# Performance work log

Measured on AMD Instinct MI355X. Metric: run time of the kernel, lower is better.

## Reference

```python
import jax, jax.numpy as jnp
import numpy as np


def setup_inputs() -> dict:
    key = jax.random.key(0)
    k1, k2 = jax.random.split(key)
    B, Ld, Lq, D = 32, 2048, 512, 256
    doc = jax.random.normal(k1, (B, Ld, D), dtype=jnp.float32)
    query = jax.random.normal(k2, (B, Lq, D), dtype=jnp.float32)
    doc_mask = jnp.ones((B, Ld), dtype=jnp.float32)
    q_mask = jnp.ones((B, Lq), dtype=jnp.float32)
    return {"doc": doc, "query": query, "doc_mask": doc_mask, "q_mask": q_mask}


def reference(doc, query, doc_mask, q_mask):
    # match_score: [B, Lq, Ld] = tanh(query @ doc^T)
    match_score = jnp.tanh(jnp.einsum('bqd,btd->bqt', query, doc))
    # sum over query positions -> [B, Ld]; softmax over doc positions
    query_to_doc_att = jax.nn.softmax(jnp.sum(match_score, axis=1), axis=-1)
    # sum over doc positions -> [B, Lq]; softmax over query positions
    doc_to_query_att = jax.nn.softmax(jnp.sum(match_score, axis=-1), axis=-1)
    # mask and renormalize
    alpha = query_to_doc_att * doc_mask
    alpha = alpha / jnp.sum(alpha, axis=1, keepdims=True)
    beta = doc_to_query_att * q_mask
    beta = beta / jnp.sum(beta, axis=1, keepdims=True)
    # weighted pooling: doc^T @ alpha -> [B, D]; query^T @ beta -> [B, D]
    doc_vector = jnp.einsum('btd,bt->bd', doc, alpha)
    que_vector = jnp.einsum('bqd,bq->bd', query, beta)
    return jnp.concatenate([doc_vector, que_vector], axis=1)  # [B, 2D]
```

## Files before the change

kernel.cpp:

```cpp
#include <hip/hip_runtime.h>
#include <hip/hip_bf16.h>
#include <cstdint>

#define BB 32
#define LD 2048
#define LQ 512
#define DD 256
#define BM 128
#define BN 128
#define BK 64

typedef _Float16 half8 __attribute__((ext_vector_type(8)));
typedef _Float16 half4 __attribute__((ext_vector_type(4)));
typedef float float4v __attribute__((ext_vector_type(4)));

__device__ __forceinline__ float tanh_fast(float x) {
    float t = __builtin_amdgcn_exp2f(x * 2.885390081777927f);
    float r = __builtin_amdgcn_rcpf(t + 1.0f);
    return fmaf(-2.0f, r, 1.0f);
}

__device__ __forceinline__ void load_lds16(const void* g, void* s) {
    __builtin_amdgcn_global_load_lds((const __attribute__((address_space(1))) void*)g,
                                     (__attribute__((address_space(3))) void*)s, 16, 0, 0);
}

#define DOCN8 (BB * LD * DD / 8)
#define QRYN8 (BB * LQ * DD / 8)

__global__ __launch_bounds__(256) void kconv(const float* __restrict__ doc,
                                             const float* __restrict__ qry,
                                             _Float16* __restrict__ dh,
                                             _Float16* __restrict__ qh) {
    int i = blockIdx.x * 256 + threadIdx.x;
    const float* src;
    _Float16* dst;
    int idx;
    if (i < DOCN8) { src = doc; dst = dh; idx = i; }
    else           { src = qry; dst = qh; idx = i - DOCN8; }
    const float4v* s = (const float4v*)src + (size_t)idx * 2;
    float4v a = s[0], c = s[1];
    half8 h = {(_Float16)a[0], (_Float16)a[1], (_Float16)a[2], (_Float16)a[3],
               (_Float16)c[0], (_Float16)c[1], (_Float16)c[2], (_Float16)c[3]};
    *((half8*)dst + idx) = h;
}

template <bool F16SRC>
__global__ __launch_bounds__(256) void k1(const void* __restrict__ qsrc,
                                          const void* __restrict__ dsrc,
                                          float* __restrict__ pa,
                                          float* __restrict__ pb) {
    __shared__ _Float16 sQ[BM * BK];
    __shared__ _Float16 sD[BN * BK];
    __shared__ float srow[BM][2];
    __shared__ float scol[BN][2];
    const int bq = blockIdx.x, bt = blockIdx.y, b = blockIdx.z;
    const int tid = threadIdx.x;
    const int lane = tid & 63;
    const int wave = tid >> 6;
    const int r16 = lane & 15;
    const int q4 = lane >> 4;
    const int mb = (wave >> 1) * 64, nb = (wave & 1) * 64;

    float4v acc[4][4];
    float4v zero = {0.f, 0.f, 0.f, 0.f};
#pragma unroll
    for (int m = 0; m < 4; m++)
#pragma unroll
        for (int n = 0; n < 4; n++) acc[m][n] = zero;

    const int lrow = lane >> 3;
    const int lcol = ((lane & 7) ^ lrow) * 8;

    for (int kk = 0; kk < DD; kk += BK) {
        __syncthreads();
        if constexpr (F16SRC) {
            const _Float16* Qh = (const _Float16*)qsrc + ((size_t)b * LQ + bq * BM) * DD;
            const _Float16* Dh = (const _Float16*)dsrc + ((size_t)b * LD + bt * BN) * DD;
#pragma unroll
            for (int j = 0; j < 4; j++) {
                int c = wave * 4 + j;
                int row = 8 * c + lrow;
                load_lds16(Qh + (size_t)row * DD + kk + lcol, &sQ[c * 512]);
                load_lds16(Dh + (size_t)row * DD + kk + lcol, &sD[c * 512]);
            }
        } else {
            const float* Qf = (const float*)qsrc + ((size_t)b * LQ + bq * BM) * DD;
            const float* Df = (const float*)dsrc + ((size_t)b * LD + bt * BN) * DD;
#pragma unroll
            for (int i = 0; i < 8; i++) {
                int f = tid + 256 * i;
                int row = f >> 4, c = f & 15;
                int c2 = c >> 1, hlf = c & 1;
                int p = c2 ^ (row & 7);
                float4v v = *(const float4v*)(Qf + (size_t)row * DD + kk + 4 * c);
                half4 h = {(_Float16)v[0], (_Float16)v[1], (_Float16)v[2], (_Float16)v[3]};
                *(half4*)(&sQ[row * BK + p * 8 + hlf * 4]) = h;
                float4v w = *(const float4v*)(Df + (size_t)row * DD + kk + 4 * c);
                half4 h2 = {(_Float16)w[0], (_Float16)w[1], (_Float16)w[2], (_Float16)w[3]};
                *(half4*)(&sD[row * BK + p * 8 + hlf * 4]) = h2;
            }
        }
        __syncthreads();

#pragma unroll
        for (int kk2 = 0; kk2 < 2; kk2++) {
            const int sw = ((4 * kk2 + q4) ^ (r16 & 7)) * 8;
            half8 af[4], bf[4];
#pragma unroll
            for (int m = 0; m < 4; m++) af[m] = *(const half8*)(&sQ[(mb + 16 * m + r16) * BK + sw]);
#pragma unroll
            for (int n = 0; n < 4; n++) bf[n] = *(const half8*)(&sD[(nb + 16 * n + r16) * BK + sw]);
#pragma unroll
            for (int m = 0; m < 4; m++)
#pragma unroll
                for (int n = 0; n < 4; n++)
                    acc[m][n] = __builtin_amdgcn_mfma_f32_16x16x32_f16(af[m], bf[n], acc[m][n], 0, 0, 0);
        }
    }

    float rsum[4][4];
    float csum[4];
#pragma unroll
    for (int m = 0; m < 4; m++)
#pragma unroll
        for (int r = 0; r < 4; r++) rsum[m][r] = 0.f;
#pragma unroll
    for (int n = 0; n < 4; n++) csum[n] = 0.f;

#pragma unroll
    for (int m = 0; m < 4; m++)
#pragma unroll
        for (int n = 0; n < 4; n++) {
            float t0 = tanh_fast(acc[m][n][0]);
            float t1 = tanh_fast(acc[m][n][1]);
            float t2 = tanh_fast(acc[m][n][2]);
            float t3 = tanh_fast(acc[m][n][3]);
            csum[n] += t0 + t1 + t2 + t3;
            rsum[m][0] += t0;
            rsum[m][1] += t1;
            rsum[m][2] += t2;
            rsum[m][3] += t3;
        }

#pragma unroll
    for (int m = 0; m < 4; m++) {
#pragma unroll
        for (int r = 0; r < 4; r++) {
            float v = rsum[m][r];
            v += __shfl_xor(v, 1);
            v += __shfl_xor(v, 2);
            v += __shfl_xor(v, 4);
            v += __shfl_xor(v, 8);
            rsum[m][r] = v;
        }
        if (r16 < 4) {
            float v = (r16 == 0) ? rsum[m][0] : (r16 == 1) ? rsum[m][1] : (r16 == 2) ? rsum[m][2] : rsum[m][3];
            srow[mb + 16 * m + 4 * q4 + r16][wave & 1] = v;
        }
    }
#pragma unroll
    for (int n = 0; n < 4; n++) {
        float v = csum[n];
        v += __shfl_xor(v, 16);
        v += __shfl_xor(v, 32);
        if (lane < 16) scol[nb + 16 * n + lane][wave >> 1] = v;
    }
    __syncthreads();
    if (tid < 128) {
        float v = srow[tid][0] + srow[tid][1];
        pb[((size_t)bt * BB + b) * LQ + bq * BM + tid] = v;
        float u = scol[tid][0] + scol[tid][1];
        pa[((size_t)bq * BB + b) * LD + bt * BN + tid] = u;
    }
}

__global__ __launch_bounds__(256) void k2(const float* __restrict__ pa, const float* __restrict__ pb,
                                          const float* __restrict__ dmask, const float* __restrict__ qmask,
                                          float* __restrict__ alpha, float* __restrict__ beta,
                                          float* __restrict__ out) {
    __shared__ float sl[2048];
    __shared__ float sm[4], ss[4];
    int blk = blockIdx.x, tid = threadIdx.x, lane = tid & 63, wave = tid >> 6;
    const float* mk;
    float* dst;
    int n;
    if (blk < BB) {
        int b = blk;
        out[b * 2 * DD + tid] = 0.f;
        out[b * 2 * DD + 256 + tid] = 0.f;
        n = LD;
        mk = dmask + b * LD;
        dst = alpha + b * LD;
        for (int i = tid; i < n; i += 256) {
            float s = 0.f;
#pragma unroll
            for (int j = 0; j < 4; j++) s += pa[((size_t)j * BB + b) * LD + i];
            sl[i] = s;
        }
    } else {
        int b = blk - BB;
        n = LQ;
        mk = qmask + b * LQ;
        dst = beta + b * LQ;
        for (int i = tid; i < n; i += 256) {
            float s = 0.f;
#pragma unroll
            for (int j = 0; j < 16; j++) s += pb[((size_t)j * BB + b) * LQ + i];
            sl[i] = s;
        }
    }
    __syncthreads();
    float mx = -3.0e38f;
    for (int i = tid; i < n; i += 256) mx = fmaxf(mx, sl[i]);
#pragma unroll
    for (int s = 1; s < 64; s <<= 1) mx = fmaxf(mx, __shfl_xor(mx, s));
    if (lane == 0) sm[wave] = mx;
    __syncthreads();
    mx = fmaxf(fmaxf(sm[0], sm[1]), fmaxf(sm[2], sm[3]));
    const float L2E = 1.4426950408889634f;
    float sum = 0.f;
    for (int i = tid; i < n; i += 256) {
        float e = __builtin_amdgcn_exp2f((sl[i] - mx) * L2E) * mk[i];
        sl[i] = e;
        sum += e;
    }
#pragma unroll
    for (int s = 1; s < 64; s <<= 1) sum += __shfl_xor(sum, s);
    if (lane == 0) ss[wave] = sum;
    __syncthreads();
    sum = ss[0] + ss[1] + ss[2] + ss[3];
    float inv = 1.0f / sum;
    for (int i = tid; i < n; i += 256) dst[i] = sl[i] * inv;
}

template <bool F16SRC>
__global__ __launch_bounds__(256) void k3(const float* __restrict__ docf, const float* __restrict__ qryf,
                                          const _Float16* __restrict__ dh, const _Float16* __restrict__ qh,
                                          const float* __restrict__ alpha, const float* __restrict__ beta,
                                          float* __restrict__ out) {
    __shared__ float sm[8 * DD];
    int blk = blockIdx.x, tid = threadIdx.x;
    const float* srcf;
    const _Float16* srch;
    const float* w;
    float* dst;
    if (blk < BB * 16) {
        int b = blk >> 4, ch = blk & 15;
        srcf = docf + ((size_t)b * LD + ch * 128) * DD;
        srch = dh + ((size_t)b * LD + ch * 128) * DD;
        w = alpha + b * LD + ch * 128;
        dst = out + b * 2 * DD;
    } else {
        int k = blk - BB * 16;
        int b = k >> 2, ch = k & 3;
        srcf = qryf + ((size_t)b * LQ + ch * 128) * DD;
        srch = qh + ((size_t)b * LQ + ch * 128) * DD;
        w = beta + b * LQ + ch * 128;
        dst = out + b * 2 * DD + DD;
    }
    int g = tid >> 5, c = tid & 31;
    float acc[8];
#pragma unroll
    for (int j = 0; j < 8; j++) acc[j] = 0.f;
#pragma unroll
    for (int r = 0; r < 16; r++) {
        int t = r * 8 + g;
        float wt = w[t];
        if constexpr (F16SRC) {
            half8 x = *(const half8*)(srch + (size_t)t * DD + c * 8);
#pragma unroll
            for (int j = 0; j < 8; j++) acc[j] += wt * (float)x[j];
        } else {
            const float4v* p = (const float4v*)(srcf + (size_t)t * DD + c * 8);
            float4v x0 = p[0], x1 = p[1];
#pragma unroll
            for (int j = 0; j < 4; j++) { acc[j] += wt * x0[j]; acc[4 + j] += wt * x1[j]; }
        }
    }
#pragma unroll
    for (int j = 0; j < 8; j++) sm[g * DD + c * 8 + j] = acc[j];
    __syncthreads();
    float s = 0.f;
#pragma unroll
    for (int g2 = 0; g2 < 8; g2++) s += sm[g2 * DD + tid];
    atomicAdd(dst + tid, s);
}

extern "C" void kernel_launch(void* const* d_in, const int* in_sizes, int n_in,
                              void* d_out, int out_size, void* d_ws, size_t ws_size,
                              hipStream_t stream) {
    (void)in_sizes; (void)n_in; (void)out_size;
    const float* doc = (const float*)d_in[0];
    const float* qry = (const float*)d_in[1];
    const float* dmask = (const float*)d_in[2];
    const float* qmask = (const float*)d_in[3];
    float* out = (float*)d_out;

    float* pa = (float*)d_ws;
    float* pb = pa + 4 * BB * LD;
    float* alpha = pb + 16 * BB * LQ;
    float* beta = alpha + BB * LD;
    _Float16* dh = (_Float16*)(beta + BB * LQ);
    _Float16* qh = dh + (size_t)BB * LD * DD;
    size_t needed = (size_t)(4 * BB * LD + 16 * BB * LQ + BB * LD + BB * LQ) * 4 +
                    ((size_t)BB * LD * DD + (size_t)BB * LQ * DD) * 2;
    bool useF16 = ws_size >= needed;

    if (useF16) {
        kconv<<<(DOCN8 + QRYN8) / 256, 256, 0, stream>>>(doc, qry, dh, qh);
        k1<true><<<dim3(LQ / BM, LD / BN, BB), 256, 0, stream>>>(qh, dh, pa, pb);
    } else {
        k1<false><<<dim3(LQ / BM, LD / BN, BB), 256, 0, stream>>>(qry, doc, pa, pb);
    }
    k2<<<2 * BB, 256, 0, stream>>>(pa, pb, dmask, qmask, alpha, beta, out);
    if (useF16) {
        k3<true><<<BB * 16 + BB * 4, 256, 0, stream>>>(doc, qry, dh, qh, alpha, beta, out);
    } else {
        k3<false><<<BB * 16 + BB * 4, 256, 0, stream>>>(doc, qry, dh, qh, alpha, beta, out);
    }
}
```

Measured before the change: 159.8 us.

## Fuse softmax and weighted pooling kernels, drop atomics, add k1 occupancy hint

Merges the softmax kernel and the pooling kernel into one. Each block recomputes the softmax for its batch row and then pools a 64-column slice of D, so alpha/beta no longer round-trip through global memory and the output zeroing and atomicAdd disappear. It also adds a min-blocks-per-CU of 4 to k1's launch bounds. In exchange, the pooling now runs on only 256 blocks, each reading a long strip of rows (2048 for doc). That lowers parallelism compared with the previous 640 blocks, and the softmax is computed redundantly four times per batch row.

```diff
diff --git a/kernel.cpp b/kernel.cpp
--- a/kernel.cpp
+++ b/kernel.cpp
@@ -46,10 +46,10 @@
 }
 
 template <bool F16SRC>
-__global__ __launch_bounds__(256) void k1(const void* __restrict__ qsrc,
-                                          const void* __restrict__ dsrc,
-                                          float* __restrict__ pa,
-                                          float* __restrict__ pb) {
+__global__ __launch_bounds__(256, 4) void k1(const void* __restrict__ qsrc,
+                                             const void* __restrict__ dsrc,
+                                             float* __restrict__ pa,
+                                             float* __restrict__ pb) {
     __shared__ _Float16 sQ[BM * BK];
     __shared__ _Float16 sD[BN * BK];
     __shared__ float srow[BM][2];
@@ -175,23 +175,23 @@
     }
 }
 
-__global__ __launch_bounds__(256) void k2(const float* __restrict__ pa, const float* __restrict__ pb,
-                                          const float* __restrict__ dmask, const float* __restrict__ qmask,
-                                          float* __restrict__ alpha, float* __restrict__ beta,
-                                          float* __restrict__ out) {
+template <bool F16SRC>
+__global__ __launch_bounds__(256) void k23(const float* __restrict__ pa, const float* __restrict__ pb,
+                                           const float* __restrict__ dmask, const float* __restrict__ qmask,
+                                           const float* __restrict__ docf, const float* __restrict__ qryf,
+                                           const _Float16* __restrict__ dh, const _Float16* __restrict__ qh,
+                                           float* __restrict__ out) {
     __shared__ float sl[2048];
+    __shared__ float sred[32][64];
     __shared__ float sm[4], ss[4];
-    int blk = blockIdx.x, tid = threadIdx.x, lane = tid & 63, wave = tid >> 6;
-    const float* mk;
-    float* dst;
-    int n;
-    if (blk < BB) {
-        int b = blk;
-        out[b * 2 * DD + tid] = 0.f;
-        out[b * 2 * DD + 256 + tid] = 0.f;
-        n = LD;
-        mk = dmask + b * LD;
-        dst = alpha + b * LD;
+    const int blk = blockIdx.x, tid = threadIdx.x, lane = tid & 63, wave = tid >> 6;
+    const bool isdoc = blk < 128;
+    const int k = isdoc ? blk : blk - 128;
+    const int b = k >> 2, dc = k & 3;
+    const int n = isdoc ? LD : LQ;
+    const float* mk = isdoc ? dmask + (size_t)b * LD : qmask + (size_t)b * LQ;
+
+    if (isdoc) {
         for (int i = tid; i < n; i += 256) {
             float s = 0.f;
 #pragma unroll
@@ -199,10 +199,6 @@
             sl[i] = s;
         }
     } else {
-        int b = blk - BB;
-        n = LQ;
-        mk = qmask + b * LQ;
-        dst = beta + b * LQ;
         for (int i = tid; i < n; i += 256) {
             float s = 0.f;
 #pragma unroll
@@ -230,61 +226,43 @@
     if (lane == 0) ss[wave] = sum;
     __syncthreads();
     sum = ss[0] + ss[1] + ss[2] + ss[3];
-    float inv = 1.0f / sum;
-    for (int i = tid; i < n; i += 256) dst[i] = sl[i] * inv;
-}
-
-template <bool F16SRC>
-__global__ __launch_bounds__(256) void k3(const float* __restrict__ docf, const float* __restrict__ qryf,
-                                          const _Float16* __restrict__ dh, const _Float16* __restrict__ qh,
-                                          const float* __restrict__ alpha, const float* __restrict__ beta,
-                                          float* __restrict__ out) {
-    __shared__ float sm[8 * DD];
-    int blk = blockIdx.x, tid = threadIdx.x;
-    const float* srcf;
-    const _Float16* srch;
-    const float* w;
-    float* dst;
-    if (blk < BB * 16) {
-        int b = blk >> 4, ch = blk & 15;
-        srcf = docf + ((size_t)b * LD + ch * 128) * DD;
-        srch = dh + ((size_t)b * LD + ch * 128) * DD;
-        w = alpha + b * LD + ch * 128;
-        dst = out + b * 2 * DD;
+    const float inv = 1.0f / sum;
+
+    const int c8 = tid & 7, pg = tid >> 3;
+    const int per = n >> 5;
+    float acc[8];
+#pragma unroll
+    for (int j = 0; j < 8; j++) acc[j] = 0.f;
+    const int dof = dc * 64 + c8 * 8;
+    if constexpr (F16SRC) {
+        const _Float16* src = (isdoc ? dh + (size_t)b * LD * DD : qh + (size_t)b * LQ * DD) + dof;
+        for (int r = 0; r < per; r++) {
+            int t = pg * per + r;
+            float wt = sl[t];
+            half8 x = *(const half8*)(src + (size_t)t * DD);
+#pragma unroll
+            for (int j = 0; j < 8; j++) acc[j] += wt * (float)x[j];
+        }
     } else {
-        int k = blk - BB * 16;
-        int b = k >> 2, ch = k & 3;
-        srcf = qryf + ((size_t)b * LQ + ch * 128) * DD;
-        srch = qh + ((size_t)b * LQ + ch * 128) * DD;
-        w = beta + b * LQ + ch * 128;
-        dst = out + b * 2 * DD + DD;
-    }
-    int g = tid >> 5, c = tid & 31;
-    float acc[8];
-#pragma unroll
-    for (int j = 0; j < 8; j++) acc[j] = 0.f;
-#pragma unroll
-    for (int r = 0; r < 16; r++) {
-        int t = r * 8 + g;
-        float wt = w[t];
-        if constexpr (F16SRC) {
-            half8 x = *(const half8*)(srch + (size_t)t * DD + c * 8);
-#pragma unroll
-            for (int j = 0; j < 8; j++) acc[j] += wt * (float)x[j];
-        } else {
-            const float4v* p = (const float4v*)(srcf + (size_t)t * DD + c * 8);
+        const float* src = (isdoc ? docf + (size_t)b * LD * DD : qryf + (size_t)b * LQ * DD) + dof;
+        for (int r = 0; r < per; r++) {
+            int t = pg * per + r;
+            float wt = sl[t];
+            const float4v* p = (const float4v*)(src + (size_t)t * DD);
             float4v x0 = p[0], x1 = p[1];
 #pragma unroll
             for (int j = 0; j < 4; j++) { acc[j] += wt * x0[j]; acc[4 + j] += wt * x1[j]; }
         }
     }
 #pragma unroll
-    for (int j = 0; j < 8; j++) sm[g * DD + c * 8 + j] = acc[j];
-    __syncthreads();
-    float s = 0.f;
-#pragma unroll
-    for (int g2 = 0; g2 < 8; g2++) s += sm[g2 * DD + tid];
-    atomicAdd(dst + tid, s);
+    for (int j = 0; j < 8; j++) sred[pg][c8 * 8 + j] = acc[j];
+    __syncthreads();
+    if (tid < 64) {
+        float s = 0.f;
+#pragma unroll
+        for (int g = 0; g < 32; g++) s += sred[g][tid];
+        out[(size_t)b * 2 * DD + (isdoc ? 0 : DD) + dc * 64 + tid] = s * inv;
+    }
 }
 
 extern "C" void kernel_launch(void* const* d_in, const int* in_sizes, int n_in,
@@ -299,24 +277,18 @@
 
     float* pa = (float*)d_ws;
     float* pb = pa + 4 * BB * LD;
-    float* alpha = pb + 16 * BB * LQ;
-    float* beta = alpha + BB * LD;
-    _Float16* dh = (_Float16*)(beta + BB * LQ);
+    _Float16* dh = (_Float16*)(pb + 16 * BB * LQ);
     _Float16* qh = dh + (size_t)BB * LD * DD;
-    size_t needed = (size_t)(4 * BB * LD + 16 * BB * LQ + BB * LD + BB * LQ) * 4 +
+    size_t needed = (size_t)(4 * BB * LD + 16 * BB * LQ) * 4 +
                     ((size_t)BB * LD * DD + (size_t)BB * LQ * DD) * 2;
     bool useF16 = ws_size >= needed;
 
     if (useF16) {
         kconv<<<(DOCN8 + QRYN8) / 256, 256, 0, stream>>>(doc, qry, dh, qh);
         k1<true><<<dim3(LQ / BM, LD / BN, BB), 256, 0, stream>>>(qh, dh, pa, pb);
+        k23<true><<<256, 256, 0, stream>>>(pa, pb, dmask, qmask, doc, qry, dh, qh, out);
     } else {
         k1<false><<<dim3(LQ / BM, LD / BN, BB), 256, 0, stream>>>(qry, doc, pa, pb);
-    }
-    k2<<<2 * BB, 256, 0, stream>>>(pa, pb, dmask, qmask, alpha, beta, out);
-    if (useF16) {
-        k3<true><<<BB * 16 + BB * 4, 256, 0, stream>>>(doc, qry, dh, qh, alpha, beta, out);
-    } else {
-        k3<false><<<BB * 16 + BB * 4, 256, 0, stream>>>(doc, qry, dh, qh, alpha, beta, out);
-    }
-}
+        k23<false><<<256, 256, 0, stream>>>(pa, pb, dmask, qmask, doc, qry, dh, qh, out);
+    }
+}
```

New measurement: 157.0 us. About the same (-1.8%).
